# Kernel tuning notes

Hardware: AMD Instinct MI355X
Metric: run time of the kernel (lower is better)

## Reference

```python
import jax, jax.numpy as jnp
import numpy as np

N = 50000      # nodes
E = 800000     # edges
IN, HID, OUT = 256, 256, 128
FCH = 32       # fc_hidden per embedding
VDIM = 2
FINAL = 2
NUM_EMB = 20


def setup_inputs() -> dict:
    key = jax.random.key(0)
    ks = jax.random.split(key, 16)
    s = 0.05
    return {
        "x": jax.random.normal(ks[0], (N, IN), jnp.float32),
        "edge_index": jax.random.randint(ks[1], (2, E), 0, N),
        "edge_cat": jax.random.randint(ks[2], (E, 2), 0, NUM_EMB),
        "edge_val": jax.random.normal(ks[3], (E, VDIM), jnp.float32),
        "W1": jax.random.normal(ks[4], (IN, HID), jnp.float32) * s,
        "b1": jnp.zeros((HID,), jnp.float32),
        "W2": jax.random.normal(ks[5], (HID, OUT), jnp.float32) * s,
        "b2": jnp.zeros((OUT,), jnp.float32),
        "emb0": jax.random.normal(ks[6], (NUM_EMB, FCH), jnp.float32) * s,
        "emb1": jax.random.normal(ks[7], (NUM_EMB, FCH), jnp.float32) * s,
        "fW1": jax.random.normal(ks[8], (OUT + 2 * FCH + VDIM, FINAL), jnp.float32) * s,
        "fb1": jnp.zeros((FINAL,), jnp.float32),
        "fW2": jax.random.normal(ks[9], (FINAL, 2), jnp.float32) * s,
        "fb2": jnp.zeros((2,), jnp.float32),
    }


def gcn_conv(h_in, W, b, src, dst, n):
    # PyG GCNConv: linear, add self-loops, symmetric D^-1/2 (A+I) D^-1/2 aggregation, bias.
    h = h_in @ W                                    # [N, F]
    ones = jnp.ones(src.shape[0], h.dtype)
    deg = jax.ops.segment_sum(ones, dst, num_segments=n) + 1.0  # +1 self-loop
    dinv = jax.lax.rsqrt(deg)                       # deg >= 1 so finite
    norm = dinv[src] * dinv[dst]                    # [E]
    agg = jax.ops.segment_sum(h[src] * norm[:, None], dst, num_segments=n)
    agg = agg + h * (dinv * dinv)[:, None]          # self-loop term, norm = dinv_i^2
    return agg + b


def reference(x, edge_index, edge_cat, edge_val,
              W1, b1, W2, b2, emb0, emb1, fW1, fb1, fW2, fb2):
    src, dst = edge_index[0], edge_index[1]
    n = x.shape[0]
    h = jax.nn.relu(gcn_conv(x, W1, b1, src, dst, n))
    h = gcn_conv(h, W2, b2, src, dst, n)            # [N, OUT]
    node2edge = h[src] - h[dst]                     # [E, OUT]
    ev = jnp.concatenate([edge_val, emb0[edge_cat[:, 0]], emb1[edge_cat[:, 1]]], axis=1)
    total = jnp.concatenate([node2edge, ev], axis=1)  # [E, OUT+2*FCH+VDIM]
    z = jax.nn.relu(total @ fW1 + fb1)              # dropout is identity in eval mode
    return z @ fW2 + fb2                            # [E, 2]
```

## Files before the change

kernel.cpp:

```cpp
#include <hip/hip_runtime.h>

#define NN 50000
#define EE 800000
#define NB ((NN + 1023) / 1024)
#define DEGB ((EE + 255) / 256)

typedef _Float16 half8v __attribute__((ext_vector_type(8)));
typedef _Float16 half4v __attribute__((ext_vector_type(4)));
typedef float f32x4 __attribute__((ext_vector_type(4)));

__global__ __launch_bounds__(256) void gemm1_mfma(const float* __restrict__ A,
                                                  const _Float16* __restrict__ BT,
                                                  const float* __restrict__ dinv,
                                                  _Float16* __restrict__ C, int M) {
    __shared__ _Float16 Ah[2][64][40];
    __shared__ _Float16 Bh[2][128][40];
    int tid = threadIdx.x;
    int bm = blockIdx.y * 64, bn = blockIdx.x * 128;
    int w = tid >> 6, l = tid & 63;
    int wr = w >> 1, wc = w & 1;
    int lr = l & 15, lg = l >> 4;
    int ar0 = tid >> 3, ac0 = tid & 7;
    int ar1 = (tid + 256) >> 3, ac1 = (tid + 256) & 7;
    int bn0 = tid >> 2, bk0 = tid & 3;
    int bn1 = (tid + 256) >> 2, bk1 = (tid + 256) & 3;
    f32x4 acc[2][4] = {};
    float4 aR0, aR1;
    half8v bR0, bR1;

    auto load_regs = [&](int k0) {
        int gm0 = bm + ar0, gm1 = bm + ar1;
        aR0 = (gm0 < M) ? *(const float4*)&A[(size_t)gm0 * 256 + k0 + ac0 * 4]
                        : make_float4(0.f, 0.f, 0.f, 0.f);
        aR1 = (gm1 < M) ? *(const float4*)&A[(size_t)gm1 * 256 + k0 + ac1 * 4]
                        : make_float4(0.f, 0.f, 0.f, 0.f);
        bR0 = *(const half8v*)&BT[(size_t)(bn + bn0) * 256 + k0 + bk0 * 8];
        bR1 = *(const half8v*)&BT[(size_t)(bn + bn1) * 256 + k0 + bk1 * 8];
    };
    auto store_lds = [&](int buf) {
        half4v h0, h1;
        h0[0] = (_Float16)aR0.x; h0[1] = (_Float16)aR0.y;
        h0[2] = (_Float16)aR0.z; h0[3] = (_Float16)aR0.w;
        h1[0] = (_Float16)aR1.x; h1[1] = (_Float16)aR1.y;
        h1[2] = (_Float16)aR1.z; h1[3] = (_Float16)aR1.w;
        *(half4v*)&Ah[buf][ar0][ac0 * 4] = h0;
        *(half4v*)&Ah[buf][ar1][ac1 * 4] = h1;
        *(half8v*)&Bh[buf][bn0][bk0 * 8] = bR0;
        *(half8v*)&Bh[buf][bn1][bk1 * 8] = bR1;
    };

    load_regs(0);
    store_lds(0);
    __syncthreads();
#pragma unroll
    for (int ks = 0; ks < 8; ++ks) {
        int cur = ks & 1;
        if (ks < 7) load_regs((ks + 1) * 32);
        half8v a[2], b[4];
#pragma unroll
        for (int mf = 0; mf < 2; ++mf)
            a[mf] = *(const half8v*)&Ah[cur][wr * 32 + mf * 16 + lr][lg * 8];
#pragma unroll
        for (int nf = 0; nf < 4; ++nf)
            b[nf] = *(const half8v*)&Bh[cur][wc * 64 + nf * 16 + lr][lg * 8];
#pragma unroll
        for (int mf = 0; mf < 2; ++mf)
#pragma unroll
            for (int nf = 0; nf < 4; ++nf)
                acc[mf][nf] = __builtin_amdgcn_mfma_f32_16x16x32_f16(a[mf], b[nf], acc[mf][nf], 0, 0, 0);
        if (ks < 7) {
            __syncthreads();
            store_lds(cur ^ 1);
            __syncthreads();
        }
    }
#pragma unroll
    for (int mf = 0; mf < 2; ++mf) {
#pragma unroll
        for (int reg = 0; reg < 4; ++reg) {
            int gr = bm + wr * 32 + mf * 16 + lg * 4 + reg;
            if (gr < M) {
                float sc = dinv[gr];
#pragma unroll
                for (int nf = 0; nf < 4; ++nf)
                    C[(size_t)gr * 256 + bn + wc * 64 + nf * 16 + lr] =
                        (_Float16)(acc[mf][nf][reg] * sc);
            }
        }
    }
}

__global__ __launch_bounds__(256) void deg_prep(const int* __restrict__ dst,
                                                int* __restrict__ deg,
                                                const float* __restrict__ W1,
                                                const float* __restrict__ W2,
                                                const float* __restrict__ fW1,
                                                const float* __restrict__ emb0,
                                                const float* __restrict__ emb1,
                                                _Float16* __restrict__ BT,
                                                float* __restrict__ Wft,
                                                float2* __restrict__ t0,
                                                float2* __restrict__ t1) {
    __shared__ float T[64][65];
    int b = blockIdx.x;
    int t = threadIdx.x;
    if (b < DEGB) {
        int e = b * 256 + t;
        if (e < EE) atomicAdd(&deg[dst[e]], 1);
    } else if (b < DEGB + 16) {
        int bb = b - DEGB;
        int k0 = (bb >> 2) * 64, n0 = (bb & 3) * 64;
#pragma unroll
        for (int i = 0; i < 16; ++i) {
            int r = i * 4 + (t >> 6), c = t & 63;
            T[r][c] = W1[(size_t)(k0 + r) * 256 + n0 + c];
        }
        __syncthreads();
#pragma unroll
        for (int i = 0; i < 16; ++i) {
            int n = i * 4 + (t >> 6), k = t & 63;
            BT[(size_t)(n0 + n) * 256 + k0 + k] = (_Float16)T[k][n];
        }
    } else {
        int k = t;
        float s0 = 0.f, s1 = 0.f;
        for (int m = 0; m < 128; ++m) {
            float wv = W2[(size_t)k * 128 + m];
            s0 += wv * fW1[m * 2 + 0];
            s1 += wv * fW1[m * 2 + 1];
        }
        Wft[k] = s0;
        Wft[256 + k] = s1;
        if (k < 20) {
            float a0 = 0.f, a1 = 0.f, b0 = 0.f, b1v = 0.f;
            for (int u = 0; u < 32; ++u) {
                float e0 = emb0[k * 32 + u], e1 = emb1[k * 32 + u];
                a0 += e0 * fW1[(130 + u) * 2 + 0];
                a1 += e0 * fW1[(130 + u) * 2 + 1];
                b0 += e1 * fW1[(162 + u) * 2 + 0];
                b1v += e1 * fW1[(162 + u) * 2 + 1];
            }
            t0[k] = make_float2(a0, a1);
            t1[k] = make_float2(b0, b1v);
        }
    }
}

__global__ __launch_bounds__(1024) void scan_partial(const int* __restrict__ deg,
                                                     int* __restrict__ rowptr,
                                                     int* __restrict__ bsum) {
    __shared__ int wsum[16];
    int tid = threadIdx.x, lane = tid & 63, w = tid >> 6;
    int idx = blockIdx.x * 1024 + tid;
    int v = (idx < NN) ? deg[idx] : 0;
    int x = v;
#pragma unroll
    for (int off = 1; off < 64; off <<= 1) {
        int t = __shfl_up(x, off, 64);
        if (lane >= off) x += t;
    }
    if (lane == 63) wsum[w] = x;
    __syncthreads();
    if (w == 0) {
        int s = (lane < 16) ? wsum[lane] : 0;
#pragma unroll
        for (int off = 1; off < 16; off <<= 1) {
            int t = __shfl_up(s, off, 64);
            if (lane >= off) s += t;
        }
        if (lane < 16) wsum[lane] = s;
    }
    __syncthreads();
    int wpre = (w == 0) ? 0 : wsum[w - 1];
    if (idx < NN) rowptr[idx] = wpre + (x - v);
    if (tid == 0) bsum[blockIdx.x] = wsum[15];
}

__global__ __launch_bounds__(64) void scan_bsum(int* __restrict__ bsum,
                                                int* __restrict__ rowptr) {
    int l = threadIdx.x;
    int v = (l < NB) ? bsum[l] : 0;
    int x = v;
#pragma unroll
    for (int off = 1; off < 64; off <<= 1) {
        int t = __shfl_up(x, off, 64);
        if (l >= off) x += t;
    }
    if (l < NB) bsum[l] = x - v;
    if (l == NB - 1) rowptr[NN] = x;
}

__global__ void scan_add_dinv(int* __restrict__ rowptr, const int* __restrict__ bsum,
                              const int* __restrict__ deg, float* __restrict__ dinv) {
    int idx = blockIdx.x * blockDim.x + threadIdx.x;
    if (idx < NN) {
        rowptr[idx] += bsum[idx >> 10];
        dinv[idx] = rsqrtf((float)deg[idx] + 1.0f);
    }
}

__global__ void fill_csr(const int* __restrict__ src, const int* __restrict__ dst,
                         const int* __restrict__ rowptr, int* __restrict__ cursor,
                         int* __restrict__ csr_src) {
    int e = blockIdx.x * blockDim.x + threadIdx.x;
    if (e >= EE) return;
    int d = dst[e];
    int pos = atomicAdd(&cursor[d], 1);
    csr_src[rowptr[d] + pos] = src[e];
}

__global__ __launch_bounds__(256) void gather_project(const _Float16* __restrict__ hs,
                                                      const int* __restrict__ rowptr,
                                                      const int* __restrict__ csr_src,
                                                      const float* __restrict__ dinv,
                                                      const float* __restrict__ b1,
                                                      const float* __restrict__ Wft,
                                                      float2* __restrict__ q) {
    int i = blockIdx.x * 4 + (threadIdx.x >> 6);
    int l = threadIdx.x & 63;
    int lf = l & 31, le = l >> 5;
    if (i >= NN) return;
    int start = rowptr[i], end = rowptr[i + 1];
    float acc[8] = {};
    int j = start;
    for (; j + 7 < end; j += 8) {
        int s0 = csr_src[j + 0 + le];
        int s1 = csr_src[j + 2 + le];
        int s2 = csr_src[j + 4 + le];
        int s3 = csr_src[j + 6 + le];
        half8v v0 = *(const half8v*)(hs + (size_t)s0 * 256 + lf * 8);
        half8v v1 = *(const half8v*)(hs + (size_t)s1 * 256 + lf * 8);
        half8v v2 = *(const half8v*)(hs + (size_t)s2 * 256 + lf * 8);
        half8v v3 = *(const half8v*)(hs + (size_t)s3 * 256 + lf * 8);
#pragma unroll
        for (int u = 0; u < 8; ++u)
            acc[u] += ((float)v0[u] + (float)v1[u]) + ((float)v2[u] + (float)v3[u]);
    }
    for (; j + le < end; j += 2) {
        int s = csr_src[j + le];
        half8v v = *(const half8v*)(hs + (size_t)s * 256 + lf * 8);
#pragma unroll
        for (int u = 0; u < 8; ++u) acc[u] += (float)v[u];
    }
#pragma unroll
    for (int u = 0; u < 8; ++u) acc[u] += __shfl_xor(acc[u], 32, 64);
    float di = dinv[i];
    half8v sv = *(const half8v*)(hs + (size_t)i * 256 + lf * 8);
    float q0 = 0.f, q1 = 0.f;
#pragma unroll
    for (int u = 0; u < 8; ++u) {
        float o = fmaxf((acc[u] + (float)sv[u]) * di + b1[lf * 8 + u], 0.f);
        q0 += o * Wft[lf * 8 + u];
        q1 += o * Wft[256 + lf * 8 + u];
    }
#pragma unroll
    for (int off = 16; off > 0; off >>= 1) {
        q0 += __shfl_xor(q0, off, 64);
        q1 += __shfl_xor(q1, off, 64);
    }
    if (l == 0) q[i] = make_float2(q0 * di, q1 * di);
}

__global__ __launch_bounds__(256) void gather_gn(const float2* __restrict__ q,
                                                 const int* __restrict__ rowptr,
                                                 const int* __restrict__ csr_src,
                                                 const float* __restrict__ dinv,
                                                 float2* __restrict__ gn) {
    int i = blockIdx.x * blockDim.x + threadIdx.x;
    if (i >= NN) return;
    int start = rowptr[i], end = rowptr[i + 1];
    float a0 = 0.f, a1 = 0.f;
    for (int j = start; j < end; ++j) {
        float2 v = q[csr_src[j]];
        a0 += v.x;
        a1 += v.y;
    }
    float2 self = q[i];
    float di = dinv[i];
    gn[i] = make_float2((a0 + self.x) * di, (a1 + self.y) * di);
}

__global__ __launch_bounds__(256) void edge_out(const float2* __restrict__ gn,
                                                const int* __restrict__ src,
                                                const int* __restrict__ dst,
                                                const int2* __restrict__ ecat,
                                                const float2* __restrict__ ev,
                                                const float* __restrict__ fW1,
                                                const float2* __restrict__ t0,
                                                const float2* __restrict__ t1,
                                                const float* __restrict__ fb1,
                                                const float* __restrict__ fW2,
                                                const float* __restrict__ fb2,
                                                float2* __restrict__ out) {
    int e = blockIdx.x * blockDim.x + threadIdx.x;
    if (e >= EE) return;
    int s = src[e], d = dst[e];
    float2 gs = gn[s], gd = gn[d];
    int2 c = ecat[e];
    float2 v = ev[e];
    float2 e0 = t0[c.x], e1 = t1[c.y];
    float z0 = gs.x - gd.x + v.x * fW1[128 * 2 + 0] + v.y * fW1[129 * 2 + 0] + e0.x + e1.x;
    float z1 = gs.y - gd.y + v.x * fW1[128 * 2 + 1] + v.y * fW1[129 * 2 + 1] + e0.y + e1.y;
    float y0 = fmaxf(z0 + fb1[0], 0.f);
    float y1 = fmaxf(z1 + fb1[1], 0.f);
    out[e] = make_float2(y0 * fW2[0] + y1 * fW2[2] + fb2[0],
                         y0 * fW2[1] + y1 * fW2[3] + fb2[1]);
}

extern "C" void kernel_launch(void* const* d_in, const int* in_sizes, int n_in,
                              void* d_out, int out_size, void* d_ws, size_t ws_size,
                              hipStream_t stream) {
    const float* x    = (const float*)d_in[0];
    const int*   eidx = (const int*)d_in[1];
    const int*   src  = eidx;
    const int*   dst  = eidx + EE;
    const int*   ecat = (const int*)d_in[2];
    const float* ev   = (const float*)d_in[3];
    const float* W1   = (const float*)d_in[4];
    const float* b1   = (const float*)d_in[5];
    const float* W2   = (const float*)d_in[6];
    const float* emb0 = (const float*)d_in[8];
    const float* emb1 = (const float*)d_in[9];
    const float* fW1  = (const float*)d_in[10];
    const float* fb1  = (const float*)d_in[11];
    const float* fW2  = (const float*)d_in[12];
    const float* fb2  = (const float*)d_in[13];
    float* out = (float*)d_out;

    char* ws = (char*)d_ws;
    size_t off = 0;
    auto alloc = [&](size_t bytes) {
        void* p = ws + off;
        off = (off + bytes + 255) & ~(size_t)255;
        return p;
    };
    int*      deg     = (int*)alloc((size_t)NN * 4);
    int*      cursor  = (int*)alloc((size_t)NN * 4);
    float*    dinv    = (float*)alloc((size_t)NN * 4);
    int*      rowptr  = (int*)alloc((size_t)(NN + 1) * 4);
    int*      bsum    = (int*)alloc((size_t)NB * 4);
    int*      csr_src = (int*)alloc((size_t)EE * 4);
    _Float16* W1T     = (_Float16*)alloc((size_t)256 * 256 * 2);
    _Float16* h1s     = (_Float16*)alloc((size_t)NN * 256 * 2);
    float2*   q       = (float2*)alloc((size_t)NN * 8);
    float2*   gn      = (float2*)alloc((size_t)NN * 8);
    float*    Wft     = (float*)alloc(512 * 4);
    float2*   t0      = (float2*)alloc(20 * 8);
    float2*   t1      = (float2*)alloc(20 * 8);

    hipMemsetAsync(deg, 0, (size_t)((char*)cursor - (char*)deg) + (size_t)NN * 4, stream);

    deg_prep<<<DEGB + 17, 256, 0, stream>>>(dst, deg, W1, W2, fW1, emb0, emb1,
                                            W1T, Wft, t0, t1);
    scan_partial<<<NB, 1024, 0, stream>>>(deg, rowptr, bsum);
    scan_bsum<<<1, 64, 0, stream>>>(bsum, rowptr);
    scan_add_dinv<<<(NN + 255) / 256, 256, 0, stream>>>(rowptr, bsum, deg, dinv);
    fill_csr<<<(EE + 255) / 256, 256, 0, stream>>>(src, dst, rowptr, cursor, csr_src);

    {
        dim3 g(2, (NN + 63) / 64);
        gemm1_mfma<<<g, 256, 0, stream>>>(x, W1T, dinv, h1s, NN);
    }
    gather_project<<<(NN + 3) / 4, 256, 0, stream>>>(
        h1s, rowptr, csr_src, dinv, b1, Wft, q);
    gather_gn<<<(NN + 255) / 256, 256, 0, stream>>>(q, rowptr, csr_src, dinv, gn);
    edge_out<<<(EE + 255) / 256, 256, 0, stream>>>(
        gn, src, dst, (const int2*)ecat, (const float2*)ev,
        fW1, t0, t1, fb1, fW2, fb2, (float2*)out);
}
```

Before: 201.5 us.

## Split hidden features into column chunks for cache-friendly neighbor gathers

The GEMM output is stored as 8 column-chunk tables of 32 features each, so every chunk table (about 3.2 MB) can stay resident in L2 while the gather runs. The gather kernel assigns one 32-lane group per (node, chunk), computes a partial projection onto the two final weights, and writes per-chunk partials. A new reduce kernel sums the partials and applies dinv. This trades wide 16-byte loads for 2-byte scalar loads and adds an extra kernel plus partial buffer traffic, in exchange for better cache locality of the random gathers.

Result: slower. 254.5 us (+26.3%).

```diff
diff --git a/kernel.cpp b/kernel.cpp
--- a/kernel.cpp
+++ b/kernel.cpp
@@ -4,6 +4,8 @@
 #define EE 800000
 #define NB ((NN + 1023) / 1024)
 #define DEGB ((EE + 255) / 256)
+#define NCH 8
+#define CHW 32
 
 typedef _Float16 half8v __attribute__((ext_vector_type(8)));
 typedef _Float16 half4v __attribute__((ext_vector_type(4)));
@@ -82,9 +84,12 @@
             if (gr < M) {
                 float sc = dinv[gr];
 #pragma unroll
-                for (int nf = 0; nf < 4; ++nf)
-                    C[(size_t)gr * 256 + bn + wc * 64 + nf * 16 + lr] =
-                        (_Float16)(acc[mf][nf][reg] * sc);
+                for (int nf = 0; nf < 4; ++nf) {
+                    int gcol = bn + wc * 64 + nf * 16 + lr;
+                    size_t cidx = (size_t)(gcol >> 5) * ((size_t)NN * CHW) +
+                                  (size_t)gr * CHW + (gcol & 31);
+                    C[cidx] = (_Float16)(acc[mf][nf][reg] * sc);
+                }
             }
         }
     }
@@ -209,56 +214,62 @@
     csr_src[rowptr[d] + pos] = src[e];
 }
 
-__global__ __launch_bounds__(256) void gather_project(const _Float16* __restrict__ hs,
-                                                      const int* __restrict__ rowptr,
-                                                      const int* __restrict__ csr_src,
-                                                      const float* __restrict__ dinv,
-                                                      const float* __restrict__ b1,
-                                                      const float* __restrict__ Wft,
-                                                      float2* __restrict__ q) {
-    int i = blockIdx.x * 4 + (threadIdx.x >> 6);
-    int l = threadIdx.x & 63;
-    int lf = l & 31, le = l >> 5;
+__global__ __launch_bounds__(256) void gather_chunks(const _Float16* __restrict__ hs,
+                                                     const int* __restrict__ rowptr,
+                                                     const int* __restrict__ csr_src,
+                                                     const float* __restrict__ dinv,
+                                                     const float* __restrict__ b1,
+                                                     const float* __restrict__ Wft,
+                                                     float2* __restrict__ qpart) {
+    int c = blockIdx.x & 7;
+    int g = blockIdx.x >> 3;
+    int half = threadIdx.x >> 5;
+    int f = threadIdx.x & 31;
+    int i = g * 8 + half;
+    const _Float16* tab = hs + (size_t)c * NN * CHW;
+    int start = rowptr[i], end = rowptr[i + 1];
+    float acc = 0.f;
+    int j = start;
+    for (; j + 3 < end; j += 4) {
+        int s0 = csr_src[j + 0];
+        int s1 = csr_src[j + 1];
+        int s2 = csr_src[j + 2];
+        int s3 = csr_src[j + 3];
+        float v0 = (float)tab[(size_t)s0 * CHW + f];
+        float v1 = (float)tab[(size_t)s1 * CHW + f];
+        float v2 = (float)tab[(size_t)s2 * CHW + f];
+        float v3 = (float)tab[(size_t)s3 * CHW + f];
+        acc += (v0 + v1) + (v2 + v3);
+    }
+    for (; j < end; ++j)
+        acc += (float)tab[(size_t)csr_src[j] * CHW + f];
+    float di = dinv[i];
+    float self = (float)tab[(size_t)i * CHW + f];
+    int fb = c * CHW + f;
+    float o = fmaxf((acc + self) * di + b1[fb], 0.f);
+    float q0 = o * Wft[fb];
+    float q1 = o * Wft[256 + fb];
+#pragma unroll
+    for (int m = 16; m > 0; m >>= 1) {
+        q0 += __shfl_xor(q0, m, 32);
+        q1 += __shfl_xor(q1, m, 32);
+    }
+    if (f == 0) qpart[(size_t)c * NN + i] = make_float2(q0, q1);
+}
+
+__global__ void reduce_q(const float2* __restrict__ qpart, const float* __restrict__ dinv,
+                         float2* __restrict__ q) {
+    int i = blockIdx.x * blockDim.x + threadIdx.x;
     if (i >= NN) return;
-    int start = rowptr[i], end = rowptr[i + 1];
-    float acc[8] = {};
-    int j = start;
-    for (; j + 7 < end; j += 8) {
-        int s0 = csr_src[j + 0 + le];
-        int s1 = csr_src[j + 2 + le];
-        int s2 = csr_src[j + 4 + le];
-        int s3 = csr_src[j + 6 + le];
-        half8v v0 = *(const half8v*)(hs + (size_t)s0 * 256 + lf * 8);
-        half8v v1 = *(const half8v*)(hs + (size_t)s1 * 256 + lf * 8);
-        half8v v2 = *(const half8v*)(hs + (size_t)s2 * 256 + lf * 8);
-        half8v v3 = *(const half8v*)(hs + (size_t)s3 * 256 + lf * 8);
-#pragma unroll
-        for (int u = 0; u < 8; ++u)
-            acc[u] += ((float)v0[u] + (float)v1[u]) + ((float)v2[u] + (float)v3[u]);
-    }
-    for (; j + le < end; j += 2) {
-        int s = csr_src[j + le];
-        half8v v = *(const half8v*)(hs + (size_t)s * 256 + lf * 8);
-#pragma unroll
-        for (int u = 0; u < 8; ++u) acc[u] += (float)v[u];
-    }
-#pragma unroll
-    for (int u = 0; u < 8; ++u) acc[u] += __shfl_xor(acc[u], 32, 64);
+    float a = 0.f, b = 0.f;
+#pragma unroll
+    for (int c = 0; c < NCH; ++c) {
+        float2 v = qpart[(size_t)c * NN + i];
+        a += v.x;
+        b += v.y;
+    }
     float di = dinv[i];
-    half8v sv = *(const half8v*)(hs + (size_t)i * 256 + lf * 8);
-    float q0 = 0.f, q1 = 0.f;
-#pragma unroll
-    for (int u = 0; u < 8; ++u) {
-        float o = fmaxf((acc[u] + (float)sv[u]) * di + b1[lf * 8 + u], 0.f);
-        q0 += o * Wft[lf * 8 + u];
-        q1 += o * Wft[256 + lf * 8 + u];
-    }
-#pragma unroll
-    for (int off = 16; off > 0; off >>= 1) {
-        q0 += __shfl_xor(q0, off, 64);
-        q1 += __shfl_xor(q1, off, 64);
-    }
-    if (l == 0) q[i] = make_float2(q0 * di, q1 * di);
+    q[i] = make_float2(a * di, b * di);
 }
 
 __global__ __launch_bounds__(256) void gather_gn(const float2* __restrict__ q,
@@ -342,6 +353,7 @@
     int*      csr_src = (int*)alloc((size_t)EE * 4);
     _Float16* W1T     = (_Float16*)alloc((size_t)256 * 256 * 2);
     _Float16* h1s     = (_Float16*)alloc((size_t)NN * 256 * 2);
+    float2*   qpart   = (float2*)alloc((size_t)NCH * NN * 8);
     float2*   q       = (float2*)alloc((size_t)NN * 8);
     float2*   gn      = (float2*)alloc((size_t)NN * 8);
     float*    Wft     = (float*)alloc(512 * 4);
@@ -361,8 +373,8 @@
         dim3 g(2, (NN + 63) / 64);
         gemm1_mfma<<<g, 256, 0, stream>>>(x, W1T, dinv, h1s, NN);
     }
-    gather_project<<<(NN + 3) / 4, 256, 0, stream>>>(
-        h1s, rowptr, csr_src, dinv, b1, Wft, q);
+    gather_chunks<<<NCH * (NN / 8), 256, 0, stream>>>(h1s, rowptr, csr_src, dinv, b1, Wft, qpart);
+    reduce_q<<<(NN + 255) / 256, 256, 0, stream>>>(qpart, dinv, q);
     gather_gn<<<(NN + 255) / 256, 256, 0, stream>>>(q, rowptr, csr_src, dinv, gn);
     edge_out<<<(EE + 255) / 256, 256, 0, stream>>>(
         gn, src, dst, (const int2*)ecat, (const float2*)ev,
```

## Fuse degree counting into GEMM launch and move dinv scaling to gather

Applied to the files above, without the earlier changes.

The GEMM no longer depends on dinv. Its output stays unscaled, and dinv[src] is applied inside the gather instead. Because of that, the degree-count atomics can run as extra blocks of the same launch as the GEMM. The atomicAdd return value is saved per edge (epos), so fill_csr needs no second atomic pass and the cursor array is removed. scan_bsum is folded into scan_add_dinv. The change costs an extra 3.2MB epos array plus per-edge dinv loads in the gather, in exchange for fewer launches and overlap of atomics with the GEMM.

New measurement: 165.2 us. 1.22x faster.

```diff
diff --git a/kernel.cpp b/kernel.cpp
--- a/kernel.cpp
+++ b/kernel.cpp
@@ -4,19 +4,77 @@
 #define EE 800000
 #define NB ((NN + 1023) / 1024)
 #define DEGB ((EE + 255) / 256)
+#define GEMMB (2 * ((NN + 63) / 64))
 
 typedef _Float16 half8v __attribute__((ext_vector_type(8)));
 typedef _Float16 half4v __attribute__((ext_vector_type(4)));
 typedef float f32x4 __attribute__((ext_vector_type(4)));
 
-__global__ __launch_bounds__(256) void gemm1_mfma(const float* __restrict__ A,
-                                                  const _Float16* __restrict__ BT,
-                                                  const float* __restrict__ dinv,
-                                                  _Float16* __restrict__ C, int M) {
+__global__ __launch_bounds__(256) void prep(const float* __restrict__ W1,
+                                            const float* __restrict__ W2,
+                                            const float* __restrict__ fW1,
+                                            const float* __restrict__ emb0,
+                                            const float* __restrict__ emb1,
+                                            _Float16* __restrict__ BT,
+                                            float* __restrict__ Wft,
+                                            float2* __restrict__ t0,
+                                            float2* __restrict__ t1) {
+    int b = blockIdx.x;
+    int t = threadIdx.x;
+    if (b < 16) {
+        __shared__ float T[64][65];
+        int k0 = (b >> 2) * 64, n0 = (b & 3) * 64;
+#pragma unroll
+        for (int i = 0; i < 16; ++i) {
+            int r = i * 4 + (t >> 6), c = t & 63;
+            T[r][c] = W1[(size_t)(k0 + r) * 256 + n0 + c];
+        }
+        __syncthreads();
+#pragma unroll
+        for (int i = 0; i < 16; ++i) {
+            int n = i * 4 + (t >> 6), k = t & 63;
+            BT[(size_t)(n0 + n) * 256 + k0 + k] = (_Float16)T[k][n];
+        }
+    } else {
+        int k = t;
+        float s0 = 0.f, s1 = 0.f;
+        for (int m = 0; m < 128; ++m) {
+            float wv = W2[(size_t)k * 128 + m];
+            s0 += wv * fW1[m * 2 + 0];
+            s1 += wv * fW1[m * 2 + 1];
+        }
+        Wft[k] = s0;
+        Wft[256 + k] = s1;
+        if (k < 20) {
+            float a0 = 0.f, a1 = 0.f, b0 = 0.f, b1v = 0.f;
+            for (int u = 0; u < 32; ++u) {
+                float e0 = emb0[k * 32 + u], e1 = emb1[k * 32 + u];
+                a0 += e0 * fW1[(130 + u) * 2 + 0];
+                a1 += e0 * fW1[(130 + u) * 2 + 1];
+                b0 += e1 * fW1[(162 + u) * 2 + 0];
+                b1v += e1 * fW1[(162 + u) * 2 + 1];
+            }
+            t0[k] = make_float2(a0, a1);
+            t1[k] = make_float2(b0, b1v);
+        }
+    }
+}
+
+__global__ __launch_bounds__(256) void gemm_deg(const float* __restrict__ A,
+                                                const _Float16* __restrict__ BT,
+                                                _Float16* __restrict__ C, int M,
+                                                const int* __restrict__ dst,
+                                                int* __restrict__ deg,
+                                                int* __restrict__ epos) {
+    if (blockIdx.x >= GEMMB) {
+        int e = (blockIdx.x - GEMMB) * 256 + threadIdx.x;
+        if (e < EE) epos[e] = atomicAdd(&deg[dst[e]], 1);
+        return;
+    }
     __shared__ _Float16 Ah[2][64][40];
     __shared__ _Float16 Bh[2][128][40];
     int tid = threadIdx.x;
-    int bm = blockIdx.y * 64, bn = blockIdx.x * 128;
+    int bm = (blockIdx.x >> 1) * 64, bn = (blockIdx.x & 1) * 128;
     int w = tid >> 6, l = tid & 63;
     int wr = w >> 1, wc = w & 1;
     int lr = l & 15, lg = l >> 4;
@@ -80,68 +138,11 @@
         for (int reg = 0; reg < 4; ++reg) {
             int gr = bm + wr * 32 + mf * 16 + lg * 4 + reg;
             if (gr < M) {
-                float sc = dinv[gr];
 #pragma unroll
                 for (int nf = 0; nf < 4; ++nf)
                     C[(size_t)gr * 256 + bn + wc * 64 + nf * 16 + lr] =
-                        (_Float16)(acc[mf][nf][reg] * sc);
+                        (_Float16)acc[mf][nf][reg];
             }
-        }
-    }
-}
-
-__global__ __launch_bounds__(256) void deg_prep(const int* __restrict__ dst,
-                                                int* __restrict__ deg,
-                                                const float* __restrict__ W1,
-                                                const float* __restrict__ W2,
-                                                const float* __restrict__ fW1,
-                                                const float* __restrict__ emb0,
-                                                const float* __restrict__ emb1,
-                                                _Float16* __restrict__ BT,
-                                                float* __restrict__ Wft,
-                                                float2* __restrict__ t0,
-                                                float2* __restrict__ t1) {
-    __shared__ float T[64][65];
-    int b = blockIdx.x;
-    int t = threadIdx.x;
-    if (b < DEGB) {
-        int e = b * 256 + t;
-        if (e < EE) atomicAdd(&deg[dst[e]], 1);
-    } else if (b < DEGB + 16) {
-        int bb = b - DEGB;
-        int k0 = (bb >> 2) * 64, n0 = (bb & 3) * 64;
-#pragma unroll
-        for (int i = 0; i < 16; ++i) {
-            int r = i * 4 + (t >> 6), c = t & 63;
-            T[r][c] = W1[(size_t)(k0 + r) * 256 + n0 + c];
-        }
-        __syncthreads();
-#pragma unroll
-        for (int i = 0; i < 16; ++i) {
-            int n = i * 4 + (t >> 6), k = t & 63;
-            BT[(size_t)(n0 + n) * 256 + k0 + k] = (_Float16)T[k][n];
-        }
-    } else {
-        int k = t;
-        float s0 = 0.f, s1 = 0.f;
-        for (int m = 0; m < 128; ++m) {
-            float wv = W2[(size_t)k * 128 + m];
-            s0 += wv * fW1[m * 2 + 0];
-            s1 += wv * fW1[m * 2 + 1];
-        }
-        Wft[k] = s0;
-        Wft[256 + k] = s1;
-        if (k < 20) {
-            float a0 = 0.f, a1 = 0.f, b0 = 0.f, b1v = 0.f;
-            for (int u = 0; u < 32; ++u) {
-                float e0 = emb0[k * 32 + u], e1 = emb1[k * 32 + u];
-                a0 += e0 * fW1[(130 + u) * 2 + 0];
-                a1 += e0 * fW1[(130 + u) * 2 + 1];
-                b0 += e1 * fW1[(162 + u) * 2 + 0];
-                b1v += e1 * fW1[(162 + u) * 2 + 1];
-            }
-            t0[k] = make_float2(a0, a1);
-            t1[k] = make_float2(b0, b1v);
         }
     }
 }
@@ -176,37 +177,39 @@
     if (tid == 0) bsum[blockIdx.x] = wsum[15];
 }
 
-__global__ __launch_bounds__(64) void scan_bsum(int* __restrict__ bsum,
-                                                int* __restrict__ rowptr) {
-    int l = threadIdx.x;
-    int v = (l < NB) ? bsum[l] : 0;
-    int x = v;
-#pragma unroll
-    for (int off = 1; off < 64; off <<= 1) {
-        int t = __shfl_up(x, off, 64);
-        if (l >= off) x += t;
-    }
-    if (l < NB) bsum[l] = x - v;
-    if (l == NB - 1) rowptr[NN] = x;
-}
-
-__global__ void scan_add_dinv(int* __restrict__ rowptr, const int* __restrict__ bsum,
-                              const int* __restrict__ deg, float* __restrict__ dinv) {
-    int idx = blockIdx.x * blockDim.x + threadIdx.x;
+__global__ __launch_bounds__(256) void scan_add_dinv(int* __restrict__ rowptr,
+                                                     const int* __restrict__ bsum,
+                                                     const int* __restrict__ deg,
+                                                     float* __restrict__ dinv) {
+    __shared__ int pre[NB + 1];
+    int t = threadIdx.x;
+    if (t < 64) {
+        int v = (t < NB) ? bsum[t] : 0;
+        int x = v;
+#pragma unroll
+        for (int o = 1; o < 64; o <<= 1) {
+            int y = __shfl_up(x, o, 64);
+            if (t >= o) x += y;
+        }
+        if (t < NB) pre[t] = x - v;
+        if (t == NB - 1) pre[NB] = x;
+    }
+    __syncthreads();
+    int idx = blockIdx.x * 256 + t;
     if (idx < NN) {
-        rowptr[idx] += bsum[idx >> 10];
+        rowptr[idx] += pre[idx >> 10];
         dinv[idx] = rsqrtf((float)deg[idx] + 1.0f);
     }
+    if (blockIdx.x == 0 && t == 0) rowptr[NN] = pre[NB];
 }
 
 __global__ void fill_csr(const int* __restrict__ src, const int* __restrict__ dst,
-                         const int* __restrict__ rowptr, int* __restrict__ cursor,
+                         const int* __restrict__ rowptr, const int* __restrict__ epos,
                          int* __restrict__ csr_src) {
     int e = blockIdx.x * blockDim.x + threadIdx.x;
     if (e >= EE) return;
     int d = dst[e];
-    int pos = atomicAdd(&cursor[d], 1);
-    csr_src[rowptr[d] + pos] = src[e];
+    csr_src[rowptr[d] + epos[e]] = src[e];
 }
 
 __global__ __launch_bounds__(256) void gather_project(const _Float16* __restrict__ hs,
@@ -228,19 +231,22 @@
         int s1 = csr_src[j + 2 + le];
         int s2 = csr_src[j + 4 + le];
         int s3 = csr_src[j + 6 + le];
+        float d0 = dinv[s0], d1 = dinv[s1], d2 = dinv[s2], d3 = dinv[s3];
         half8v v0 = *(const half8v*)(hs + (size_t)s0 * 256 + lf * 8);
         half8v v1 = *(const half8v*)(hs + (size_t)s1 * 256 + lf * 8);
         half8v v2 = *(const half8v*)(hs + (size_t)s2 * 256 + lf * 8);
         half8v v3 = *(const half8v*)(hs + (size_t)s3 * 256 + lf * 8);
 #pragma unroll
         for (int u = 0; u < 8; ++u)
-            acc[u] += ((float)v0[u] + (float)v1[u]) + ((float)v2[u] + (float)v3[u]);
+            acc[u] += (d0 * (float)v0[u] + d1 * (float)v1[u]) +
+                      (d2 * (float)v2[u] + d3 * (float)v3[u]);
     }
     for (; j + le < end; j += 2) {
         int s = csr_src[j + le];
+        float ds = dinv[s];
         half8v v = *(const half8v*)(hs + (size_t)s * 256 + lf * 8);
 #pragma unroll
-        for (int u = 0; u < 8; ++u) acc[u] += (float)v[u];
+        for (int u = 0; u < 8; ++u) acc[u] += ds * (float)v[u];
     }
 #pragma unroll
     for (int u = 0; u < 8; ++u) acc[u] += __shfl_xor(acc[u], 32, 64);
@@ -249,7 +255,7 @@
     float q0 = 0.f, q1 = 0.f;
 #pragma unroll
     for (int u = 0; u < 8; ++u) {
-        float o = fmaxf((acc[u] + (float)sv[u]) * di + b1[lf * 8 + u], 0.f);
+        float o = fmaxf((acc[u] + di * (float)sv[u]) * di + b1[lf * 8 + u], 0.f);
         q0 += o * Wft[lf * 8 + u];
         q1 += o * Wft[256 + lf * 8 + u];
     }
@@ -335,10 +341,10 @@
         return p;
     };
     int*      deg     = (int*)alloc((size_t)NN * 4);
-    int*      cursor  = (int*)alloc((size_t)NN * 4);
     float*    dinv    = (float*)alloc((size_t)NN * 4);
     int*      rowptr  = (int*)alloc((size_t)(NN + 1) * 4);
     int*      bsum    = (int*)alloc((size_t)NB * 4);
+    int*      epos    = (int*)alloc((size_t)EE * 4);
     int*      csr_src = (int*)alloc((size_t)EE * 4);
     _Float16* W1T     = (_Float16*)alloc((size_t)256 * 256 * 2);
     _Float16* h1s     = (_Float16*)alloc((size_t)NN * 256 * 2);
@@ -348,23 +354,21 @@
     float2*   t0      = (float2*)alloc(20 * 8);
     float2*   t1      = (float2*)alloc(20 * 8);
 
-    hipMemsetAsync(deg, 0, (size_t)((char*)cursor - (char*)deg) + (size_t)NN * 4, stream);
-
-    deg_prep<<<DEGB + 17, 256, 0, stream>>>(dst, deg, W1, W2, fW1, emb0, emb1,
-                                            W1T, Wft, t0, t1);
+    hipMemsetAsync(deg, 0, (size_t)NN * 4, stream);
+
+    prep<<<17, 256, 0, stream>>>(W1, W2, fW1, emb0, emb1, W1T, Wft, t0, t1);
+
+    gemm_deg<<<GEMMB + DEGB, 256, 0, stream>>>(x, W1T, h1s, NN, dst, deg, epos);
+
     scan_partial<<<NB, 1024, 0, stream>>>(deg, rowptr, bsum);
-    scan_bsum<<<1, 64, 0, stream>>>(bsum, rowptr);
     scan_add_dinv<<<(NN + 255) / 256, 256, 0, stream>>>(rowptr, bsum, deg, dinv);
-    fill_csr<<<(EE + 255) / 256, 256, 0, stream>>>(src, dst, rowptr, cursor, csr_src);
-
-    {
-        dim3 g(2, (NN + 63) / 64);
-        gemm1_mfma<<<g, 256, 0, stream>>>(x, W1T, dinv, h1s, NN);
-    }
+
+    fill_csr<<<DEGB, 256, 0, stream>>>(src, dst, rowptr, epos, csr_src);
+
     gather_project<<<(NN + 3) / 4, 256, 0, stream>>>(
         h1s, rowptr, csr_src, dinv, b1, Wft, q);
     gather_gn<<<(NN + 255) / 256, 256, 0, stream>>>(q, rowptr, csr_src, dinv, gn);
-    edge_out<<<(EE + 255) / 256, 256, 0, stream>>>(
+    edge_out<<<DEGB, 256, 0, stream>>>(
         gn, src, dst, (const int2*)ecat, (const float2*)ev,
         fW1, t0, t1, fb1, fW2, fb2, (float2*)out);
 }
```
